# Kernel optimization log

Hardware: AMD Instinct MI355X
Metric: run time of the kernel (lower is better)

The kernel has to match this reference:

```python
import jax, jax.numpy as jnp
import numpy as np

N = 50000      # nodes
E = 800000     # edges (before self loops)
F_DIM = 512    # raw feature dim
HID = 64       # hidden dim (= per-head dim, concat=False)
HEADS = 4
EMB = 64
NEG_SLOPE = 0.2
LN_EPS = 1e-5


def setup_inputs() -> dict:
    key = jax.random.key(0)
    ks = jax.random.split(key, 24)
    rn = lambda k, shape: jax.random.normal(k, shape, dtype=jnp.float32) * 0.05
    inp = {
        'features': jax.random.normal(ks[0], (N, F_DIM), dtype=jnp.float32),
        'edge_index': jax.random.randint(ks[1], (2, E), 0, N),
        'Wt': rn(ks[2], (F_DIM, HID)), 'bt': jnp.zeros((HID,), jnp.float32),
        'Wp': rn(ks[3], (HID, EMB)), 'bp': jnp.zeros((EMB,), jnp.float32),
    }
    for l in range(2):
        o = 4 + l * 4
        inp[f'Wg{l}'] = rn(ks[o], (HID, HEADS * HID))
        inp[f'as{l}'] = rn(ks[o + 1], (HEADS, HID))
        inp[f'ad{l}'] = rn(ks[o + 2], (HEADS, HID))
        inp[f'bg{l}'] = jnp.zeros((HID,), jnp.float32)
        inp[f'g{l}'] = jnp.ones((HID,), jnp.float32)
        inp[f'b{l}'] = jnp.zeros((HID,), jnp.float32)
        inp[f'a{l}'] = jnp.full((1,), 0.25, jnp.float32)  # PReLU weight
    return inp


def gat_block(x, src, dst, Wg, a_src, a_dst, bg, gamma, beta, prelu_a):
    # GATConv (heads=HEADS, concat=False, add_self_loops already in src/dst)
    h = (x @ Wg).reshape(N, HEADS, HID)                    # [N,H,C]
    al_s = jnp.einsum('nhc,hc->nh', h, a_src)              # [N,H]
    al_d = jnp.einsum('nhc,hc->nh', h, a_dst)
    e = jax.nn.leaky_relu(al_s[src] + al_d[dst], NEG_SLOPE)  # [E,H]
    m = jax.ops.segment_max(e, dst, num_segments=N)
    ex = jnp.exp(e - m[dst])
    denom = jax.ops.segment_sum(ex, dst, num_segments=N)
    alpha = ex / denom[dst]                                # segment softmax over in-edges
    out = jax.ops.segment_sum(h[src] * alpha[:, :, None], dst, num_segments=N)  # [N,H,C]
    out = out.mean(axis=1) + bg                            # concat=False -> mean heads
    # LayerNorm
    mu = out.mean(-1, keepdims=True)
    var = ((out - mu) ** 2).mean(-1, keepdims=True)
    xn = (out - mu) / jnp.sqrt(var + LN_EPS) * gamma + beta
    # PReLU
    return jnp.where(xn > 0, xn, prelu_a * xn)


def reference(features, edge_index, Wt, bt, Wp, bp,
              Wg0, as0, ad0, bg0, g0, b0, a0,
              Wg1, as1, ad1, bg1, g1, b1, a1):
    loops = jnp.arange(N)
    src = jnp.concatenate([edge_index[0], loops])
    dst = jnp.concatenate([edge_index[1], loops])
    x = features @ Wt + bt
    x = x + gat_block(x, src, dst, Wg0, as0, ad0, bg0, g0, b0, a0)
    x = x + gat_block(x, src, dst, Wg1, as1, ad1, bg1, g1, b1, a1)
    z = x @ Wp + bp
    return z / jnp.maximum(jnp.linalg.norm(z, axis=-1, keepdims=True), 1e-12)
```

## Files before the change

### kernel.cpp

```cpp
#include <hip/hip_runtime.h>
#include <hip/hip_bf16.h>

typedef __attribute__((ext_vector_type(8))) short bvec8;
typedef __attribute__((ext_vector_type(4))) float fvec4;

__device__ __forceinline__ void splitf(float f, short& hi, short& lo) {
  __hip_bfloat16 h = __float2bfloat16(f);
  float r = f - __bfloat162float(h);
  __hip_bfloat16 l = __float2bfloat16(r);
  hi = *(short*)&h;
  lo = *(short*)&l;
}
__device__ __forceinline__ float bits2f(unsigned short u) {
  unsigned int v = ((unsigned int)u) << 16;
  return __uint_as_float(v);
}

__global__ void k_degree(const int* __restrict__ ei, int* __restrict__ cnt, int E, int N) {
  int i = blockIdx.x * 256 + threadIdx.x;
  if (i >= E + N) return;
  int d = (i < E) ? ei[E + i] : (i - E);
  atomicAdd(&cnt[d], 1);
}

__global__ __launch_bounds__(1024) void k_scan_blk(const int* __restrict__ cnt, int* __restrict__ off,
                                                   int* __restrict__ bsum, int N) {
  __shared__ int wsum[16];
  int t = threadIdx.x, lane = t & 63, wv = t >> 6;
  int idx = blockIdx.x * 4096 + t * 4;
  int4 v = make_int4(0, 0, 0, 0);
  if (idx < N) v = *(const int4*)(cnt + idx);
  int s0 = v.x, s1 = s0 + v.y, s2 = s1 + v.z, s3 = s2 + v.w;
  int sc = s3;
  #pragma unroll
  for (int d = 1; d < 64; d <<= 1) {
    int u = __shfl_up(sc, d, 64);
    if (lane >= d) sc += u;
  }
  if (lane == 63) wsum[wv] = sc;
  __syncthreads();
  int woff = 0;
  #pragma unroll
  for (int w = 0; w < 16; ++w) woff += (w < wv) ? wsum[w] : 0;
  int eb = woff + sc - s3;
  if (idx < N) {
    int4 o = make_int4(eb, eb + s0, eb + s1, eb + s2);
    *(int4*)(off + idx) = o;
  }
  if (t == 1023) bsum[blockIdx.x] = woff + sc;
}

__global__ __launch_bounds__(1024) void k_scan_add(int* __restrict__ off, int* __restrict__ cur,
                                                   const int* __restrict__ bsum, int total, int N) {
  int t = threadIdx.x;
  if (blockIdx.x == 0 && t == 0) off[N] = total;
  int b = 0;
  for (int i = 0; i < blockIdx.x; ++i) b += bsum[i];
  int idx = blockIdx.x * 4096 + t * 4;
  if (idx >= N) return;
  int4 o = *(const int4*)(off + idx);
  o.x += b; o.y += b; o.z += b; o.w += b;
  *(int4*)(off + idx) = o;
  *(int4*)(cur + idx) = o;
}

__global__ void k_scatter(const int* __restrict__ ei, int* __restrict__ cur, int* __restrict__ csr, int E, int N) {
  int i = blockIdx.x * 256 + threadIdx.x;
  if (i >= E + N) return;
  int s, d;
  if (i < E) { s = ei[i]; d = ei[E + i]; } else { s = i - E; d = i - E; }
  int p = atomicAdd(&cur[d], 1);
  csr[p] = s;
}

__global__ __launch_bounds__(64) void k_prep(const float* __restrict__ Wg0, const float* __restrict__ Wg1,
                                             const float* __restrict__ Wt,
                                             short* __restrict__ pk0, short* __restrict__ pk1,
                                             short* __restrict__ wtpk) {
  int b = blockIdx.x;
  int lane = threadIdx.x;
  int fq = lane >> 4, fr = lane & 15;
  bvec8 hv, lv;
  if (b < 64) {
    const float* Wg = (b < 32) ? Wg0 : Wg1;
    short* pk = (b < 32) ? pk0 : pk1;
    int tile = b & 31;
    int w = tile >> 3, s = (tile >> 2) & 1, ct = tile & 3;
    #pragma unroll
    for (int j = 0; j < 8; ++j) {
      short hh, ll;
      splitf(Wg[(size_t)(s * 32 + fq * 8 + j) * 256 + w * 64 + ct * 16 + fr], hh, ll);
      hv[j] = hh; lv[j] = ll;
    }
    *(bvec8*)(pk + tile * 1024 + lane * 8) = hv;
    *(bvec8*)(pk + tile * 1024 + 512 + lane * 8) = lv;
  } else {
    int tile = b - 64;
    int s = tile >> 2, nt = tile & 3;
    #pragma unroll
    for (int j = 0; j < 8; ++j) {
      short hh, ll;
      splitf(Wt[(size_t)(s * 32 + fq * 8 + j) * 64 + nt * 16 + fr], hh, ll);
      hv[j] = hh; lv[j] = ll;
    }
    *(bvec8*)(wtpk + tile * 1024 + lane * 8) = hv;
    *(bvec8*)(wtpk + tile * 1024 + 512 + lane * 8) = lv;
  }
}

__global__ __launch_bounds__(256) void k_x0(const float* __restrict__ feat, const short* __restrict__ wtpk,
                                            const float* __restrict__ bt,
                                            short* __restrict__ xhi, short* __restrict__ xlo, int N) {
  const int t = threadIdx.x;
  const int lane = t & 63;
  const int w = t >> 6;
  const int fr = lane & 15;
  const int fq = lane >> 4;
  const int n0 = blockIdx.x * 128;

  int ar0 = n0 + w * 32 + fr;      if (ar0 >= N) ar0 = N - 1;
  int ar1 = n0 + w * 32 + 16 + fr; if (ar1 >= N) ar1 = N - 1;
  const float* fb0 = feat + (size_t)ar0 * 512 + fq * 8;
  const float* fb1 = feat + (size_t)ar1 * 512 + fq * 8;

  fvec4 acc[2][4];
  #pragma unroll
  for (int m = 0; m < 2; ++m)
    #pragma unroll
    for (int nt = 0; nt < 4; ++nt) acc[m][nt] = (fvec4){0.f, 0.f, 0.f, 0.f};

  for (int s = 0; s < 16; ++s) {
    bvec8 bh[4], bl[4];
    #pragma unroll
    for (int nt = 0; nt < 4; ++nt) {
      bh[nt] = *(const bvec8*)(wtpk + (s * 4 + nt) * 1024 + lane * 8);
      bl[nt] = *(const bvec8*)(wtpk + (s * 4 + nt) * 1024 + 512 + lane * 8);
    }
    #pragma unroll
    for (int m = 0; m < 2; ++m) {
      const float* fb = m ? fb1 : fb0;
      float4 f0 = *(const float4*)(fb + s * 32);
      float4 f1 = *(const float4*)(fb + s * 32 + 4);
      float fv[8] = {f0.x, f0.y, f0.z, f0.w, f1.x, f1.y, f1.z, f1.w};
      bvec8 ah, al;
      #pragma unroll
      for (int j = 0; j < 8; ++j) { short hh, ll; splitf(fv[j], hh, ll); ah[j] = hh; al[j] = ll; }
      #pragma unroll
      for (int nt = 0; nt < 4; ++nt) {
        acc[m][nt] = __builtin_amdgcn_mfma_f32_16x16x32_bf16(ah, bh[nt], acc[m][nt], 0, 0, 0);
        acc[m][nt] = __builtin_amdgcn_mfma_f32_16x16x32_bf16(ah, bl[nt], acc[m][nt], 0, 0, 0);
        acc[m][nt] = __builtin_amdgcn_mfma_f32_16x16x32_bf16(al, bh[nt], acc[m][nt], 0, 0, 0);
      }
    }
  }
  #pragma unroll
  for (int m = 0; m < 2; ++m)
    #pragma unroll
    for (int nt = 0; nt < 4; ++nt) {
      float btv = bt[nt * 16 + fr];
      #pragma unroll
      for (int r = 0; r < 4; ++r) {
        int node = n0 + w * 32 + m * 16 + fq * 4 + r;
        if (node < N) {
          short hh, ll;
          splitf(acc[m][nt][r] + btv, hh, ll);
          xhi[(size_t)node * 64 + nt * 16 + fr] = hh;
          xlo[(size_t)node * 64 + nt * 16 + fr] = ll;
        }
      }
    }
}

__global__ __launch_bounds__(256) void k_h(const short* __restrict__ xhi, const short* __restrict__ xlo,
                                           const short* __restrict__ pk,
                                           const float* __restrict__ as_, const float* __restrict__ ad_,
                                           __hip_bfloat16* __restrict__ h, float* __restrict__ als,
                                           float* __restrict__ ald, int N) {
  const int t = threadIdx.x;
  const int lane = t & 63;
  const int w = t >> 6;
  const int fr = lane & 15;
  const int fq = lane >> 4;
  const int n0 = blockIdx.x * 64;

  bvec8 bh[2][4], bl[2][4];
  #pragma unroll
  for (int s = 0; s < 2; ++s)
    #pragma unroll
    for (int ct = 0; ct < 4; ++ct) {
      int tile = (w * 2 + s) * 4 + ct;
      bh[s][ct] = *(const bvec8*)(pk + tile * 1024 + lane * 8);
      bl[s][ct] = *(const bvec8*)(pk + tile * 1024 + 512 + lane * 8);
    }
  fvec4 acc[4][4];
  #pragma unroll
  for (int nt = 0; nt < 4; ++nt)
    #pragma unroll
    for (int ct = 0; ct < 4; ++ct) acc[nt][ct] = (fvec4){0.f, 0.f, 0.f, 0.f};
  #pragma unroll
  for (int nt = 0; nt < 4; ++nt) {
    int row = n0 + nt * 16 + fr; if (row >= N) row = N - 1;
    const short* xh = xhi + (size_t)row * 64 + fq * 8;
    const short* xl = xlo + (size_t)row * 64 + fq * 8;
    #pragma unroll
    for (int s = 0; s < 2; ++s) {
      const bvec8 ah = *(const bvec8*)(xh + s * 32);
      const bvec8 al = *(const bvec8*)(xl + s * 32);
      #pragma unroll
      for (int ct = 0; ct < 4; ++ct) {
        acc[nt][ct] = __builtin_amdgcn_mfma_f32_16x16x32_bf16(ah, bh[s][ct], acc[nt][ct], 0, 0, 0);
        acc[nt][ct] = __builtin_amdgcn_mfma_f32_16x16x32_bf16(ah, bl[s][ct], acc[nt][ct], 0, 0, 0);
        acc[nt][ct] = __builtin_amdgcn_mfma_f32_16x16x32_bf16(al, bh[s][ct], acc[nt][ct], 0, 0, 0);
      }
    }
  }
  float asv[4], adv[4];
  #pragma unroll
  for (int ct = 0; ct < 4; ++ct) {
    asv[ct] = as_[w * 64 + ct * 16 + fr];
    adv[ct] = ad_[w * 64 + ct * 16 + fr];
  }
  #pragma unroll
  for (int nt = 0; nt < 4; ++nt) {
    #pragma unroll
    for (int r = 0; r < 4; ++r) {
      int n = n0 + nt * 16 + fq * 4 + r;
      float ps = 0.f, pd = 0.f;
      #pragma unroll
      for (int ct = 0; ct < 4; ++ct) {
        ps = fmaf(acc[nt][ct][r], asv[ct], ps);
        pd = fmaf(acc[nt][ct][r], adv[ct], pd);
      }
      #pragma unroll
      for (int m = 1; m < 16; m <<= 1) { ps += __shfl_xor(ps, m, 64); pd += __shfl_xor(pd, m, 64); }
      if (fr == 0 && n < N) { als[(size_t)n * 4 + w] = ps; ald[(size_t)n * 4 + w] = pd; }
      #pragma unroll
      for (int ct = 0; ct < 4; ++ct)
        if (n < N) h[(size_t)n * 256 + w * 64 + ct * 16 + fr] = __float2bfloat16(acc[nt][ct][r]);
    }
  }
}

template <bool FINAL>
__global__ __launch_bounds__(1024) void k_agg(const unsigned short* __restrict__ hb, const float* __restrict__ als,
                                              const float* __restrict__ ald, const int* __restrict__ off,
                                              const int* __restrict__ csr, const float* __restrict__ bg,
                                              const float* __restrict__ gam, const float* __restrict__ bet,
                                              const float* __restrict__ pa,
                                              short* __restrict__ xhi, short* __restrict__ xlo,
                                              const float* __restrict__ Wp, const float* __restrict__ bp,
                                              float* __restrict__ out, int N) {
  int lane = threadIdx.x & 63;
  int n = blockIdx.x * 16 + (threadIdx.x >> 6);
  if (n >= N) return;
  int hh = lane >> 4;
  int cg = (lane & 15) * 4;
  float aldv = ald[(size_t)n * 4 + hh];
  int e0 = __builtin_amdgcn_readfirstlane(off[n]);
  int e1 = __builtin_amdgcn_readfirstlane(off[n + 1]);
  float a0 = 0, a1 = 0, a2 = 0, a3 = 0, den = 0;
  const int co = hh * 64 + cg;
  int e = e0;
  for (; e + 4 <= e1; e += 4) {
    int s0 = csr[e + 0], s1 = csr[e + 1], s2 = csr[e + 2], s3 = csr[e + 3];
    float q0 = als[(size_t)s0 * 4 + hh];
    float q1 = als[(size_t)s1 * 4 + hh];
    float q2 = als[(size_t)s2 * 4 + hh];
    float q3 = als[(size_t)s3 * 4 + hh];
    ushort4 g0 = *(const ushort4*)(hb + (size_t)s0 * 256 + co);
    ushort4 g1 = *(const ushort4*)(hb + (size_t)s1 * 256 + co);
    ushort4 g2 = *(const ushort4*)(hb + (size_t)s2 * 256 + co);
    ushort4 g3 = *(const ushort4*)(hb + (size_t)s3 * 256 + co);
    float t0 = q0 + aldv; t0 = fmaxf(t0, 0.2f * t0); float w0 = __expf(t0);
    float t1 = q1 + aldv; t1 = fmaxf(t1, 0.2f * t1); float w1 = __expf(t1);
    float t2 = q2 + aldv; t2 = fmaxf(t2, 0.2f * t2); float w2 = __expf(t2);
    float t3 = q3 + aldv; t3 = fmaxf(t3, 0.2f * t3); float w3 = __expf(t3);
    den += (w0 + w1) + (w2 + w3);
    a0 += w0 * bits2f(g0.x) + w1 * bits2f(g1.x) + w2 * bits2f(g2.x) + w3 * bits2f(g3.x);
    a1 += w0 * bits2f(g0.y) + w1 * bits2f(g1.y) + w2 * bits2f(g2.y) + w3 * bits2f(g3.y);
    a2 += w0 * bits2f(g0.z) + w1 * bits2f(g1.z) + w2 * bits2f(g2.z) + w3 * bits2f(g3.z);
    a3 += w0 * bits2f(g0.w) + w1 * bits2f(g1.w) + w2 * bits2f(g2.w) + w3 * bits2f(g3.w);
  }
  for (; e < e1; ++e) {
    int s = csr[e];
    float t = als[(size_t)s * 4 + hh] + aldv;
    t = fmaxf(t, 0.2f * t);
    float w = __expf(t);
    den += w;
    const ushort4 hv = *(const ushort4*)(hb + (size_t)s * 256 + co);
    a0 += w * bits2f(hv.x); a1 += w * bits2f(hv.y); a2 += w * bits2f(hv.z); a3 += w * bits2f(hv.w);
  }
  float inv = 1.0f / den;
  a0 *= inv; a1 *= inv; a2 *= inv; a3 *= inv;
  a0 += __shfl_xor(a0, 16, 64); a0 += __shfl_xor(a0, 32, 64);
  a1 += __shfl_xor(a1, 16, 64); a1 += __shfl_xor(a1, 32, 64);
  a2 += __shfl_xor(a2, 16, 64); a2 += __shfl_xor(a2, 32, 64);
  a3 += __shfl_xor(a3, 16, 64); a3 += __shfl_xor(a3, 32, 64);
  float v0 = a0 * 0.25f + bg[cg + 0];
  float v1 = a1 * 0.25f + bg[cg + 1];
  float v2 = a2 * 0.25f + bg[cg + 2];
  float v3 = a3 * 0.25f + bg[cg + 3];
  float sum = v0 + v1 + v2 + v3;
  #pragma unroll
  for (int m = 1; m < 16; m <<= 1) sum += __shfl_xor(sum, m, 64);
  float mu = sum * (1.f / 64.f);
  float d0 = v0 - mu, d1 = v1 - mu, d2 = v2 - mu, d3 = v3 - mu;
  float vv = d0 * d0 + d1 * d1 + d2 * d2 + d3 * d3;
  #pragma unroll
  for (int m = 1; m < 16; m <<= 1) vv += __shfl_xor(vv, m, 64);
  float rstd = rsqrtf(vv * (1.f / 64.f) + 1e-5f);
  float A = pa[0];
  float y0 = d0 * rstd * gam[cg + 0] + bet[cg + 0];
  float y1 = d1 * rstd * gam[cg + 1] + bet[cg + 1];
  float y2 = d2 * rstd * gam[cg + 2] + bet[cg + 2];
  float y3 = d3 * rstd * gam[cg + 3] + bet[cg + 3];
  y0 = y0 > 0.f ? y0 : A * y0;
  y1 = y1 > 0.f ? y1 : A * y1;
  y2 = y2 > 0.f ? y2 : A * y2;
  y3 = y3 > 0.f ? y3 : A * y3;
  float o0 = 0.f, o1 = 0.f, o2 = 0.f, o3 = 0.f;
  if (lane < 16) {
    ushort4 xh = *(const ushort4*)((const unsigned short*)xhi + (size_t)n * 64 + cg);
    ushort4 xl = *(const ushort4*)((const unsigned short*)xlo + (size_t)n * 64 + cg);
    o0 = bits2f(xh.x) + bits2f(xl.x) + y0;
    o1 = bits2f(xh.y) + bits2f(xl.y) + y1;
    o2 = bits2f(xh.z) + bits2f(xl.z) + y2;
    o3 = bits2f(xh.w) + bits2f(xl.w) + y3;
  }
  if (!FINAL) {
    if (lane < 16) {
      short h0, l0, h1, l1, h2, l2, h3, l3;
      splitf(o0, h0, l0); splitf(o1, h1, l1); splitf(o2, h2, l2); splitf(o3, h3, l3);
      ushort4 oh = make_ushort4((unsigned short)h0, (unsigned short)h1, (unsigned short)h2, (unsigned short)h3);
      ushort4 ol = make_ushort4((unsigned short)l0, (unsigned short)l1, (unsigned short)l2, (unsigned short)l3);
      *(ushort4*)((unsigned short*)xhi + (size_t)n * 64 + cg) = oh;
      *(ushort4*)((unsigned short*)xlo + (size_t)n * 64 + cg) = ol;
    }
  } else {
    float acc = bp[lane];
    #pragma unroll
    for (int g = 0; g < 16; ++g) {
      float rx = __shfl(o0, g, 64), ry = __shfl(o1, g, 64);
      float rz = __shfl(o2, g, 64), rw = __shfl(o3, g, 64);
      const float* wp = Wp + g * 4 * 64 + lane;
      acc = fmaf(rx, wp[0],   acc);
      acc = fmaf(ry, wp[64],  acc);
      acc = fmaf(rz, wp[128], acc);
      acc = fmaf(rw, wp[192], acc);
    }
    float sq = acc * acc;
    #pragma unroll
    for (int m = 1; m < 64; m <<= 1) sq += __shfl_xor(sq, m, 64);
    float nrm = fmaxf(sqrtf(sq), 1e-12f);
    out[(size_t)n * 64 + lane] = acc / nrm;
  }
}

extern "C" void kernel_launch(void* const* d_in, const int* in_sizes, int n_in,
                              void* d_out, int out_size, void* d_ws, size_t ws_size,
                              hipStream_t stream) {
  const float* feat = (const float*)d_in[0];
  const int*   ei   = (const int*)d_in[1];
  const float* Wt   = (const float*)d_in[2];
  const float* bt   = (const float*)d_in[3];
  const float* Wp   = (const float*)d_in[4];
  const float* bp   = (const float*)d_in[5];
  const float* Wg[2]  = {(const float*)d_in[6],  (const float*)d_in[13]};
  const float* as_[2] = {(const float*)d_in[7],  (const float*)d_in[14]};
  const float* ad_[2] = {(const float*)d_in[8],  (const float*)d_in[15]};
  const float* bg[2]  = {(const float*)d_in[9],  (const float*)d_in[16]};
  const float* gm[2]  = {(const float*)d_in[10], (const float*)d_in[17]};
  const float* be[2]  = {(const float*)d_in[11], (const float*)d_in[18]};
  const float* pa[2]  = {(const float*)d_in[12], (const float*)d_in[19]};

  const int N = in_sizes[0] / 512;
  const int E = in_sizes[1] / 2;

  short* xhi = (short*)d_ws;
  short* xlo = xhi + (size_t)N * 64;
  __hip_bfloat16* hb = (__hip_bfloat16*)(xlo + (size_t)N * 64);
  float* als = (float*)((short*)hb + (size_t)N * 256);
  float* ald = als + (size_t)N * 4;
  int* cnt = (int*)(ald + (size_t)N * 4);
  int* cur = cnt + N;
  int* csr = cur + N;
  int* off = csr + (E + N);
  int* bsum = off + (N + 1);
  short* pk0 = (short*)(((uintptr_t)(bsum + 16) + 15) & ~(uintptr_t)15);
  short* pk1 = pk0 + 32768;
  short* wtpk = pk1 + 32768;

  hipMemsetAsync(cnt, 0, (size_t)N * sizeof(int), stream);
  int eb = (E + N + 255) / 256;
  int SB = (N + 4095) / 4096;
  k_degree<<<eb, 256, 0, stream>>>(ei, cnt, E, N);
  k_prep<<<128, 64, 0, stream>>>(Wg[0], Wg[1], Wt, pk0, pk1, wtpk);
  k_scan_blk<<<SB, 1024, 0, stream>>>(cnt, off, bsum, N);
  k_scan_add<<<SB, 1024, 0, stream>>>(off, cur, bsum, E + N, N);
  k_scatter<<<eb, 256, 0, stream>>>(ei, cur, csr, E, N);

  int nb16 = (N + 15) / 16;
  int nb64 = (N + 63) / 64;
  int nb128 = (N + 127) / 128;
  k_x0<<<nb128, 256, 0, stream>>>(feat, wtpk, bt, xhi, xlo, N);

  k_h<<<nb64, 256, 0, stream>>>(xhi, xlo, pk0, as_[0], ad_[0], (__hip_bfloat16*)hb, als, ald, N);
  k_agg<false><<<nb16, 1024, 0, stream>>>((const unsigned short*)hb, als, ald, off, csr, bg[0], gm[0], be[0], pa[0],
                                          xhi, xlo, Wp, bp, (float*)d_out, N);
  k_h<<<nb64, 256, 0, stream>>>(xhi, xlo, pk1, as_[1], ad_[1], (__hip_bfloat16*)hb, als, ald, N);
  k_agg<true><<<nb16, 1024, 0, stream>>>((const unsigned short*)hb, als, ald, off, csr, bg[1], gm[1], be[1], pa[1],
                                         xhi, xlo, Wp, bp, (float*)d_out, N);
}
```

Baseline: 491.7 us.

## Fuse input projection with first GAT transform, single-block scan, smaller agg blocks

Merges the feature projection (k_x0) with the first layer's head transform and attention-logit computation (k_h) into one kernel, staging x in shared memory so it is not reread from global memory. It also replaces the two-kernel block scan with a single-block sequential scan that writes off and cur together. The memset is folded into k_prep, and aggregation blocks shrink from 1024 to 256 threads. Together these cut launches and an intermediate round trip. The cost is a fully serial scan over roughly a dozen chunks and smaller 64-row blocks for the 512-wide projection.

```diff
diff --git a/kernel.cpp b/kernel.cpp
--- a/kernel.cpp
+++ b/kernel.cpp
@@ -23,45 +23,41 @@
   atomicAdd(&cnt[d], 1);
 }
 
-__global__ __launch_bounds__(1024) void k_scan_blk(const int* __restrict__ cnt, int* __restrict__ off,
-                                                   int* __restrict__ bsum, int N) {
+__global__ __launch_bounds__(1024) void k_scan(const int* __restrict__ cnt, int* __restrict__ off,
+                                               int* __restrict__ cur, int N) {
   __shared__ int wsum[16];
+  __shared__ int s_carry;
   int t = threadIdx.x, lane = t & 63, wv = t >> 6;
-  int idx = blockIdx.x * 4096 + t * 4;
-  int4 v = make_int4(0, 0, 0, 0);
-  if (idx < N) v = *(const int4*)(cnt + idx);
-  int s0 = v.x, s1 = s0 + v.y, s2 = s1 + v.z, s3 = s2 + v.w;
-  int sc = s3;
-  #pragma unroll
-  for (int d = 1; d < 64; d <<= 1) {
-    int u = __shfl_up(sc, d, 64);
-    if (lane >= d) sc += u;
-  }
-  if (lane == 63) wsum[wv] = sc;
+  if (t == 0) s_carry = 0;
   __syncthreads();
-  int woff = 0;
-  #pragma unroll
-  for (int w = 0; w < 16; ++w) woff += (w < wv) ? wsum[w] : 0;
-  int eb = woff + sc - s3;
-  if (idx < N) {
-    int4 o = make_int4(eb, eb + s0, eb + s1, eb + s2);
-    *(int4*)(off + idx) = o;
-  }
-  if (t == 1023) bsum[blockIdx.x] = woff + sc;
-}
-
-__global__ __launch_bounds__(1024) void k_scan_add(int* __restrict__ off, int* __restrict__ cur,
-                                                   const int* __restrict__ bsum, int total, int N) {
-  int t = threadIdx.x;
-  if (blockIdx.x == 0 && t == 0) off[N] = total;
-  int b = 0;
-  for (int i = 0; i < blockIdx.x; ++i) b += bsum[i];
-  int idx = blockIdx.x * 4096 + t * 4;
-  if (idx >= N) return;
-  int4 o = *(const int4*)(off + idx);
-  o.x += b; o.y += b; o.z += b; o.w += b;
-  *(int4*)(off + idx) = o;
-  *(int4*)(cur + idx) = o;
+  for (int base = 0; base < N; base += 4096) {
+    int idx = base + t * 4;
+    int4 v = make_int4(0, 0, 0, 0);
+    if (idx < N) v = *(const int4*)(cnt + idx);
+    int s0 = v.x, s1 = s0 + v.y, s2 = s1 + v.z, s3 = s2 + v.w;
+    int sc = s3;
+    #pragma unroll
+    for (int d = 1; d < 64; d <<= 1) {
+      int u = __shfl_up(sc, d, 64);
+      if (lane >= d) sc += u;
+    }
+    if (lane == 63) wsum[wv] = sc;
+    __syncthreads();
+    int carry = s_carry;
+    int woff = 0;
+    #pragma unroll
+    for (int w = 0; w < 16; ++w) woff += (w < wv) ? wsum[w] : 0;
+    int eb = carry + woff + sc - s3;
+    if (idx < N) {
+      int4 o = make_int4(eb, eb + s0, eb + s1, eb + s2);
+      *(int4*)(off + idx) = o;
+      *(int4*)(cur + idx) = o;
+    }
+    __syncthreads();
+    if (t == 1023) s_carry = carry + woff + sc;
+    __syncthreads();
+  }
+  if (t == 0) off[N] = s_carry;
 }
 
 __global__ void k_scatter(const int* __restrict__ ei, int* __restrict__ cur, int* __restrict__ csr, int E, int N) {
@@ -76,9 +72,10 @@
 __global__ __launch_bounds__(64) void k_prep(const float* __restrict__ Wg0, const float* __restrict__ Wg1,
                                              const float* __restrict__ Wt,
                                              short* __restrict__ pk0, short* __restrict__ pk1,
-                                             short* __restrict__ wtpk) {
+                                             short* __restrict__ wtpk, int* __restrict__ cnt, int N) {
   int b = blockIdx.x;
   int lane = threadIdx.x;
+  for (int i = b * 64 + lane; i < N; i += 128 * 64) cnt[i] = 0;
   int fq = lane >> 4, fr = lane & 15;
   bvec8 hv, lv;
   if (b < 64) {
@@ -108,37 +105,35 @@
   }
 }
 
-__global__ __launch_bounds__(256) void k_x0(const float* __restrict__ feat, const short* __restrict__ wtpk,
-                                            const float* __restrict__ bt,
-                                            short* __restrict__ xhi, short* __restrict__ xlo, int N) {
+#define HROW 72
+__global__ __launch_bounds__(256) void k_x0h(const float* __restrict__ feat, const short* __restrict__ wtpk,
+                                             const float* __restrict__ bt, const short* __restrict__ pk,
+                                             const float* __restrict__ as_, const float* __restrict__ ad_,
+                                             short* __restrict__ xhi, short* __restrict__ xlo,
+                                             __hip_bfloat16* __restrict__ h, float* __restrict__ als,
+                                             float* __restrict__ ald, int N) {
+  __shared__ __align__(16) short sXh[64 * HROW];
+  __shared__ __align__(16) short sXl[64 * HROW];
   const int t = threadIdx.x;
   const int lane = t & 63;
   const int w = t >> 6;
   const int fr = lane & 15;
   const int fq = lane >> 4;
-  const int n0 = blockIdx.x * 128;
-
-  int ar0 = n0 + w * 32 + fr;      if (ar0 >= N) ar0 = N - 1;
-  int ar1 = n0 + w * 32 + 16 + fr; if (ar1 >= N) ar1 = N - 1;
-  const float* fb0 = feat + (size_t)ar0 * 512 + fq * 8;
-  const float* fb1 = feat + (size_t)ar1 * 512 + fq * 8;
-
-  fvec4 acc[2][4];
-  #pragma unroll
-  for (int m = 0; m < 2; ++m)
-    #pragma unroll
-    for (int nt = 0; nt < 4; ++nt) acc[m][nt] = (fvec4){0.f, 0.f, 0.f, 0.f};
-
-  for (int s = 0; s < 16; ++s) {
-    bvec8 bh[4], bl[4];
-    #pragma unroll
-    for (int nt = 0; nt < 4; ++nt) {
-      bh[nt] = *(const bvec8*)(wtpk + (s * 4 + nt) * 1024 + lane * 8);
-      bl[nt] = *(const bvec8*)(wtpk + (s * 4 + nt) * 1024 + 512 + lane * 8);
-    }
-    #pragma unroll
-    for (int m = 0; m < 2; ++m) {
-      const float* fb = m ? fb1 : fb0;
+  const int n0 = blockIdx.x * 64;
+
+  {
+    int ar = n0 + w * 16 + fr; if (ar >= N) ar = N - 1;
+    const float* fb = feat + (size_t)ar * 512 + fq * 8;
+    fvec4 acc[4];
+    #pragma unroll
+    for (int nt = 0; nt < 4; ++nt) acc[nt] = (fvec4){0.f, 0.f, 0.f, 0.f};
+    for (int s = 0; s < 16; ++s) {
+      bvec8 bh[4], bl[4];
+      #pragma unroll
+      for (int nt = 0; nt < 4; ++nt) {
+        bh[nt] = *(const bvec8*)(wtpk + (s * 4 + nt) * 1024 + lane * 8);
+        bl[nt] = *(const bvec8*)(wtpk + (s * 4 + nt) * 1024 + 512 + lane * 8);
+      }
       float4 f0 = *(const float4*)(fb + s * 32);
       float4 f1 = *(const float4*)(fb + s * 32 + 4);
       float fv[8] = {f0.x, f0.y, f0.z, f0.w, f1.x, f1.y, f1.z, f1.w};
@@ -147,28 +142,85 @@
       for (int j = 0; j < 8; ++j) { short hh, ll; splitf(fv[j], hh, ll); ah[j] = hh; al[j] = ll; }
       #pragma unroll
       for (int nt = 0; nt < 4; ++nt) {
-        acc[m][nt] = __builtin_amdgcn_mfma_f32_16x16x32_bf16(ah, bh[nt], acc[m][nt], 0, 0, 0);
-        acc[m][nt] = __builtin_amdgcn_mfma_f32_16x16x32_bf16(ah, bl[nt], acc[m][nt], 0, 0, 0);
-        acc[m][nt] = __builtin_amdgcn_mfma_f32_16x16x32_bf16(al, bh[nt], acc[m][nt], 0, 0, 0);
-      }
-    }
-  }
-  #pragma unroll
-  for (int m = 0; m < 2; ++m)
+        acc[nt] = __builtin_amdgcn_mfma_f32_16x16x32_bf16(ah, bh[nt], acc[nt], 0, 0, 0);
+        acc[nt] = __builtin_amdgcn_mfma_f32_16x16x32_bf16(ah, bl[nt], acc[nt], 0, 0, 0);
+        acc[nt] = __builtin_amdgcn_mfma_f32_16x16x32_bf16(al, bh[nt], acc[nt], 0, 0, 0);
+      }
+    }
     #pragma unroll
     for (int nt = 0; nt < 4; ++nt) {
       float btv = bt[nt * 16 + fr];
       #pragma unroll
       for (int r = 0; r < 4; ++r) {
-        int node = n0 + w * 32 + m * 16 + fq * 4 + r;
+        int row = w * 16 + fq * 4 + r;
+        short hh, ll;
+        splitf(acc[nt][r] + btv, hh, ll);
+        sXh[row * HROW + nt * 16 + fr] = hh;
+        sXl[row * HROW + nt * 16 + fr] = ll;
+        int node = n0 + row;
         if (node < N) {
-          short hh, ll;
-          splitf(acc[m][nt][r] + btv, hh, ll);
           xhi[(size_t)node * 64 + nt * 16 + fr] = hh;
           xlo[(size_t)node * 64 + nt * 16 + fr] = ll;
         }
       }
     }
+  }
+  __syncthreads();
+  bvec8 bh[2][4], bl[2][4];
+  #pragma unroll
+  for (int s = 0; s < 2; ++s)
+    #pragma unroll
+    for (int ct = 0; ct < 4; ++ct) {
+      int tile = (w * 2 + s) * 4 + ct;
+      bh[s][ct] = *(const bvec8*)(pk + tile * 1024 + lane * 8);
+      bl[s][ct] = *(const bvec8*)(pk + tile * 1024 + 512 + lane * 8);
+    }
+  fvec4 acc[4][4];
+  #pragma unroll
+  for (int nt = 0; nt < 4; ++nt)
+    #pragma unroll
+    for (int ct = 0; ct < 4; ++ct) acc[nt][ct] = (fvec4){0.f, 0.f, 0.f, 0.f};
+  #pragma unroll
+  for (int nt = 0; nt < 4; ++nt) {
+    const short* xh = sXh + (nt * 16 + fr) * HROW + fq * 8;
+    const short* xl = sXl + (nt * 16 + fr) * HROW + fq * 8;
+    #pragma unroll
+    for (int s = 0; s < 2; ++s) {
+      const bvec8 ah = *(const bvec8*)(xh + s * 32);
+      const bvec8 al = *(const bvec8*)(xl + s * 32);
+      #pragma unroll
+      for (int ct = 0; ct < 4; ++ct) {
+        acc[nt][ct] = __builtin_amdgcn_mfma_f32_16x16x32_bf16(ah, bh[s][ct], acc[nt][ct], 0, 0, 0);
+        acc[nt][ct] = __builtin_amdgcn_mfma_f32_16x16x32_bf16(ah, bl[s][ct], acc[nt][ct], 0, 0, 0);
+        acc[nt][ct] = __builtin_amdgcn_mfma_f32_16x16x32_bf16(al, bh[s][ct], acc[nt][ct], 0, 0, 0);
+      }
+    }
+  }
+  float asv[4], adv[4];
+  #pragma unroll
+  for (int ct = 0; ct < 4; ++ct) {
+    asv[ct] = as_[w * 64 + ct * 16 + fr];
+    adv[ct] = ad_[w * 64 + ct * 16 + fr];
+  }
+  #pragma unroll
+  for (int nt = 0; nt < 4; ++nt) {
+    #pragma unroll
+    for (int r = 0; r < 4; ++r) {
+      int n = n0 + nt * 16 + fq * 4 + r;
+      float ps = 0.f, pd = 0.f;
+      #pragma unroll
+      for (int ct = 0; ct < 4; ++ct) {
+        ps = fmaf(acc[nt][ct][r], asv[ct], ps);
+        pd = fmaf(acc[nt][ct][r], adv[ct], pd);
+      }
+      #pragma unroll
+      for (int m = 1; m < 16; m <<= 1) { ps += __shfl_xor(ps, m, 64); pd += __shfl_xor(pd, m, 64); }
+      if (fr == 0 && n < N) { als[(size_t)n * 4 + w] = ps; ald[(size_t)n * 4 + w] = pd; }
+      #pragma unroll
+      for (int ct = 0; ct < 4; ++ct)
+        if (n < N) h[(size_t)n * 256 + w * 64 + ct * 16 + fr] = __float2bfloat16(acc[nt][ct][r]);
+    }
+  }
 }
 
 __global__ __launch_bounds__(256) void k_h(const short* __restrict__ xhi, const short* __restrict__ xlo,
@@ -242,16 +294,16 @@
 }
 
 template <bool FINAL>
-__global__ __launch_bounds__(1024) void k_agg(const unsigned short* __restrict__ hb, const float* __restrict__ als,
-                                              const float* __restrict__ ald, const int* __restrict__ off,
-                                              const int* __restrict__ csr, const float* __restrict__ bg,
-                                              const float* __restrict__ gam, const float* __restrict__ bet,
-                                              const float* __restrict__ pa,
-                                              short* __restrict__ xhi, short* __restrict__ xlo,
-                                              const float* __restrict__ Wp, const float* __restrict__ bp,
-                                              float* __restrict__ out, int N) {
+__global__ __launch_bounds__(256) void k_agg(const unsigned short* __restrict__ hb, const float* __restrict__ als,
+                                             const float* __restrict__ ald, const int* __restrict__ off,
+                                             const int* __restrict__ csr, const float* __restrict__ bg,
+                                             const float* __restrict__ gam, const float* __restrict__ bet,
+                                             const float* __restrict__ pa,
+                                             short* __restrict__ xhi, short* __restrict__ xlo,
+                                             const float* __restrict__ Wp, const float* __restrict__ bp,
+                                             float* __restrict__ out, int N) {
   int lane = threadIdx.x & 63;
-  int n = blockIdx.x * 16 + (threadIdx.x >> 6);
+  int n = blockIdx.x * 4 + (threadIdx.x >> 6);
   if (n >= N) return;
   int hh = lane >> 4;
   int cg = (lane & 15) * 4;
@@ -385,29 +437,23 @@
   int* cur = cnt + N;
   int* csr = cur + N;
   int* off = csr + (E + N);
-  int* bsum = off + (N + 1);
-  short* pk0 = (short*)(((uintptr_t)(bsum + 16) + 15) & ~(uintptr_t)15);
+  short* pk0 = (short*)(((uintptr_t)(off + N + 1) + 15) & ~(uintptr_t)15);
   short* pk1 = pk0 + 32768;
   short* wtpk = pk1 + 32768;
 
-  hipMemsetAsync(cnt, 0, (size_t)N * sizeof(int), stream);
   int eb = (E + N + 255) / 256;
-  int SB = (N + 4095) / 4096;
+  k_prep<<<128, 64, 0, stream>>>(Wg[0], Wg[1], Wt, pk0, pk1, wtpk, cnt, N);
   k_degree<<<eb, 256, 0, stream>>>(ei, cnt, E, N);
-  k_prep<<<128, 64, 0, stream>>>(Wg[0], Wg[1], Wt, pk0, pk1, wtpk);
-  k_scan_blk<<<SB, 1024, 0, stream>>>(cnt, off, bsum, N);
-  k_scan_add<<<SB, 1024, 0, stream>>>(off, cur, bsum, E + N, N);
+  k_scan<<<1, 1024, 0, stream>>>(cnt, off, cur, N);
   k_scatter<<<eb, 256, 0, stream>>>(ei, cur, csr, E, N);
 
-  int nb16 = (N + 15) / 16;
+  int nb4 = (N + 3) / 4;
   int nb64 = (N + 63) / 64;
-  int nb128 = (N + 127) / 128;
-  k_x0<<<nb128, 256, 0, stream>>>(feat, wtpk, bt, xhi, xlo, N);
-
-  k_h<<<nb64, 256, 0, stream>>>(xhi, xlo, pk0, as_[0], ad_[0], (__hip_bfloat16*)hb, als, ald, N);
-  k_agg<false><<<nb16, 1024, 0, stream>>>((const unsigned short*)hb, als, ald, off, csr, bg[0], gm[0], be[0], pa[0],
-                                          xhi, xlo, Wp, bp, (float*)d_out, N);
+  k_x0h<<<nb64, 256, 0, stream>>>(feat, wtpk, bt, pk0, as_[0], ad_[0], xhi, xlo,
+                                  (__hip_bfloat16*)hb, als, ald, N);
+  k_agg<false><<<nb4, 256, 0, stream>>>((const unsigned short*)hb, als, ald, off, csr, bg[0], gm[0], be[0], pa[0],
+                                        xhi, xlo, Wp, bp, (float*)d_out, N);
   k_h<<<nb64, 256, 0, stream>>>(xhi, xlo, pk1, as_[1], ad_[1], (__hip_bfloat16*)hb, als, ald, N);
-  k_agg<true><<<nb16, 1024, 0, stream>>>((const unsigned short*)hb, als, ald, off, csr, bg[1], gm[1], be[1], pa[1],
-                                         xhi, xlo, Wp, bp, (float*)d_out, N);
-}
+  k_agg<true><<<nb4, 256, 0, stream>>>((const unsigned short*)hb, als, ald, off, csr, bg[1], gm[1], be[1], pa[1],
+                                       xhi, xlo, Wp, bp, (float*)d_out, N);
+}
```

Measured after the change: 486.5 us. Within noise of the previous version (-1.1%).
